# Kernel tuning notes

Hardware: AMD Instinct MI355X
Metric: run time of the kernel (lower is better)

## Reference

```python
import jax, jax.numpy as jnp
import numpy as np

N, D = 1024, 128
NEG_INF = -1e30


def setup_inputs() -> dict:
    key = jax.random.key(0)
    ks = jax.random.split(key, 8)
    s = 0.05
    return {
        "X": jax.random.normal(ks[0], (N, D), dtype=jnp.float32),
        "Wq": jax.random.normal(ks[1], (D, D), dtype=jnp.float32) * s,
        "Wk": jax.random.normal(ks[2], (D, D), dtype=jnp.float32) * s,
        "v": jax.random.normal(ks[3], (D,), dtype=jnp.float32) * s,
        "w_ih": jax.random.normal(ks[4], (3 * D, 2 * D), dtype=jnp.float32) * s,
        "w_hh": jax.random.normal(ks[5], (3 * D, D), dtype=jnp.float32) * s,
        "b_ih": jax.random.normal(ks[6], (3 * D,), dtype=jnp.float32) * s,
        "b_hh": jax.random.normal(ks[7], (3 * D,), dtype=jnp.float32) * s,
    }


def reference(X, Wq, Wk, v, w_ih, w_hh, b_ih, b_hh):
    n, d = X.shape
    # --- anti-causal additive attention (query i attends keys j >= i) ---
    q = X @ Wq.T                                   # (N, d)
    k = X @ Wk.T                                   # (N, d)
    # scores[i, j] = v . tanh(q_i + k_j)
    scores = jnp.einsum("ijd,d->ij", jnp.tanh(q[:, None, :] + k[None, :, :]), v)
    mask = jnp.arange(n)[None, :] >= jnp.arange(n)[:, None]   # suffix j >= i
    scores = jnp.where(mask, scores, NEG_INF)
    w = jax.nn.softmax(scores, axis=1)             # (N, N)
    att = w @ X                                    # (N, d) context over keys

    # --- single-layer GRU over the N "time" steps, batch 1 ---
    gru_in = jnp.concatenate((X, att), axis=1)     # (N, 2d)
    gi = gru_in @ w_ih.T + b_ih                    # (N, 3d) input gates, precomputed

    def step(h, gi_t):
        gh = h @ w_hh.T + b_hh                     # (3d,)
        i_r, i_z, i_n = jnp.split(gi_t, 3)
        h_r, h_z, h_n = jnp.split(gh, 3)
        r = jax.nn.sigmoid(i_r + h_r)
        z = jax.nn.sigmoid(i_z + h_z)
        nst = jnp.tanh(i_n + r * h_n)
        h_new = (1.0 - z) * nst + z * h
        return h_new, h_new

    h0 = jnp.zeros((d,), dtype=X.dtype)
    _, out = jax.lax.scan(step, h0, gi)            # (N, d)
    return out
```

## Files before the change

### kernel.cpp

```cpp
#include <hip/hip_runtime.h>
#include <hip/hip_bf16.h>

#define N 1024
#define D 128
#define SB 8
#define NSB (N / SB)

typedef __hip_bfloat16 bf16;
typedef __attribute__((ext_vector_type(8))) short bfx8;
typedef __attribute__((ext_vector_type(4))) float fx4;
typedef __attribute__((ext_vector_type(4))) unsigned short u16x4;

__device__ __forceinline__ float b2f(bf16 x) { return __bfloat162float(x); }
__device__ __forceinline__ short f2bf_bits(float x) {
    bf16 b = __float2bfloat16(x);
    return *reinterpret_cast<short*>(&b);
}
__device__ __forceinline__ float bfbits2f(unsigned short u) {
    return __uint_as_float(((unsigned int)u) << 16);
}
__device__ __forceinline__ float fastrcp(float x) { return __builtin_amdgcn_rcpf(x); }

__device__ __forceinline__ float fast_tanh(float x) {
    float e = __expf(2.f * x);
    return 1.f - 2.f * fastrcp(e + 1.f);
}
__device__ __forceinline__ float fast_sigmoid(float x) {
    return fastrcp(1.f + __expf(-x));
}

__device__ __forceinline__ float sel4(fx4 v, int r) {
    float x = (r & 1) ? v[1] : v[0];
    float y = (r & 1) ? v[3] : v[2];
    return (r & 2) ? y : x;
}

__device__ __forceinline__ void async_copy16(const float* g, void* l) {
    __builtin_amdgcn_global_load_lds((const __attribute__((address_space(1))) void*)g,
                                     (__attribute__((address_space(3))) void*)l, 16, 0, 0);
}

__device__ __forceinline__ void wait_rows(int* cnt, int grp) {
    while (__hip_atomic_load(&cnt[grp], __ATOMIC_ACQUIRE, __HIP_MEMORY_SCOPE_AGENT) < 8)
        __builtin_amdgcn_s_sleep(2);
}

__device__ __forceinline__ float cvt(const void* p, int idx, int isbf) {
    return isbf ? b2f(((const bf16*)p)[idx]) : ((const float*)p)[idx];
}

#define MFMA(A, B, C) __builtin_amdgcn_mfma_f32_16x16x32_bf16((A), (B), (C), 0, 0, 0)

__global__ void __launch_bounds__(256) prep_kernel(
        const void* inX, const void* inWq, const void* inWk, const void* inV,
        const void* inWih, const void* inWhh, const void* inBih, const void* inBhh,
        float* __restrict__ Xf, float* __restrict__ WqT, float* __restrict__ WkT,
        float* __restrict__ vf, float* __restrict__ wihT, float* __restrict__ whhf,
        float* __restrict__ bihf, float* __restrict__ bhhf,
        int* __restrict__ flag, int* __restrict__ cnt, int* __restrict__ rcnt) {
    __shared__ int red[256];
    int t = threadIdx.x;
    const unsigned short* xu = (const unsigned short*)inX;
    int c = 0;
#pragma unroll
    for (int k = 0; k < 4; ++k) {
        unsigned short u = xu[2 * (4 * t + k)];
        int e = (u >> 7) & 0xFF;
        c += (e >= 96 && e <= 144) ? 1 : 0;
    }
    red[t] = c;
    __syncthreads();
    for (int st = 128; st > 0; st >>= 1) {
        if (t < st) red[t] += red[t + st];
        __syncthreads();
    }
    int isbf = red[0] > 800;

    if (blockIdx.x == 0) {
        if (t == 0) *flag = isbf;
        if (t < 128) { cnt[t] = 0; rcnt[t] = 0; }
    }

    int id = blockIdx.x * 256 + t;
    if (id < 131072) {
        Xf[id] = cvt(inX, id, isbf);
    } else if (id < 147456) {
        int k = id - 131072; int cc = k >> 7, d = k & 127;
        WqT[k] = cvt(inWq, d * 128 + cc, isbf);
    } else if (id < 163840) {
        int k = id - 147456; int cc = k >> 7, d = k & 127;
        WkT[k] = cvt(inWk, d * 128 + cc, isbf);
    } else if (id < 163968) {
        vf[id - 163840] = cvt(inV, id - 163840, isbf);
    } else if (id < 262272) {
        int k = id - 163968; int cc = k / 384, o = k - cc * 384;
        wihT[k] = cvt(inWih, o * 256 + cc, isbf);
    } else if (id < 311424) {
        whhf[id - 262272] = cvt(inWhh, id - 262272, isbf);
    } else if (id < 311808) {
        bihf[id - 311424] = cvt(inBih, id - 311424, isbf);
    } else if (id < 312192) {
        bhhf[id - 311808] = cvt(inBhh, id - 311808, isbf);
    }
}

__global__ void __launch_bounds__(256) qk_gix_kernel(
        const float* __restrict__ X, const float* __restrict__ WqT,
        const float* __restrict__ WkT, const float* __restrict__ wihT,
        float* __restrict__ q, float* __restrict__ kT, float* __restrict__ gix) {
    int i = blockIdx.x, t = threadIdx.x;
    __shared__ float xs[D];
    if (t < D) xs[t] = X[i * D + t];
    __syncthreads();
    int d = t & 127;
    const float* WT = (t < 128) ? WqT : WkT;
    float acc = 0.f;
#pragma unroll 8
    for (int cc = 0; cc < D; ++cc) acc += xs[cc] * WT[cc * D + d];
    if (t < 128) q[i * D + d] = acc;
    else         kT[d * N + i] = acc;

    for (int o = t; o < 3 * D; o += 256) {
        float a2 = 0.f;
#pragma unroll 8
        for (int cc = 0; cc < D; ++cc) a2 += xs[cc] * wihT[cc * 384 + o];
        gix[i * 384 + o] = a2;
    }
}

__global__ void __launch_bounds__(256, 1) fused_kernel(
        const float* __restrict__ q, const float* __restrict__ kT,
        const float* __restrict__ v, const float* __restrict__ X,
        const float* __restrict__ wihT, const float* __restrict__ b_ih,
        const float* __restrict__ b_hh, const float* __restrict__ gix,
        float* __restrict__ gi, const float* __restrict__ w_hh,
        void* __restrict__ out, const int* __restrict__ flag,
        int* __restrict__ cnt, int* __restrict__ rcnt,
        float* __restrict__ attMS, float* __restrict__ attA) {
    __shared__ __align__(16) char smem[2 * SB * 3 * D * 4 + (SB + 1) * D * 2];
    int t = threadIdx.x;

    if (blockIdx.x != 0) {
        int b = blockIdx.x - 1;
        int i, P, p;
        if (b < 256)      { i = b >> 3;            P = 8; p = b & 7; }
        else if (b < 448) { int e = b - 256; i = 32 + (e >> 1); P = 2; p = e & 1; }
        else              { i = 128 + (b - 448);   P = 1; p = 0; }

        float* qs   = (float*)smem;
        float* vs   = qs + D;
        float* al   = vs + D;
        float* wrow = al + D;
        float* red  = wrow + N;

        int len = (N - i + P - 1) / P;
        int j0 = i + p * len;
        int j1 = min(j0 + len, N);

        if (t < D) { qs[t] = q[i * D + t]; vs[t] = v[t]; }
        __syncthreads();

        float sj[4];
        int nj = 0;
        float m = -1e30f;
        for (int j = j0 + t; j < j1; j += 256) {
            float s = 0.f;
#pragma unroll 8
            for (int dd = 0; dd < D; ++dd) s += vs[dd] * fast_tanh(qs[dd] + kT[dd * N + j]);
            sj[nj++] = s;
            m = fmaxf(m, s);
        }
        red[t] = m;
        __syncthreads();
        for (int st = 128; st > 0; st >>= 1) {
            if (t < st) red[t] = fmaxf(red[t], red[t + st]);
            __syncthreads();
        }
        m = red[0];
        __syncthreads();
        float lsum = 0.f;
        {
            int it = 0;
            for (int j = j0 + t; j < j1; j += 256, ++it) {
                float pe = __expf(sj[it] - m);
                wrow[j - j0] = pe;
                lsum += pe;
            }
        }
        red[t] = lsum;
        __syncthreads();
        for (int st = 128; st > 0; st >>= 1) {
            if (t < st) red[t] += red[t + st];
            __syncthreads();
        }
        float S = red[0];
        __syncthreads();
        int d = t & 127, half = t >> 7;
        float acc = 0.f;
        int cl = j1 - j0;
        for (int jj = half; jj < cl; jj += 2) acc += wrow[jj] * X[(j0 + jj) * D + d];
        if (half) red[d] = acc;
        __syncthreads();
        if (!half) al[d] = acc + red[d];
        __syncthreads();

        if (P > 1) {
            if (t < D) attA[(i * 8 + p) * D + t] = al[t];
            if (t == 0) { attMS[(i * 8 + p) * 2] = m; attMS[(i * 8 + p) * 2 + 1] = S; }
            __syncthreads();
            if (t == 0) {
                __threadfence();
                int arr = __hip_atomic_fetch_add(&rcnt[i], 1, __ATOMIC_ACQ_REL,
                                                 __HIP_MEMORY_SCOPE_AGENT);
                ((int*)red)[0] = arr;
            }
            __syncthreads();
            int arr = ((int*)red)[0];
            if (arr != P - 1) return;
            if (t < D) {
                float M = -1e30f;
                for (int pp = 0; pp < P; ++pp) M = fmaxf(M, attMS[(i * 8 + pp) * 2]);
                float Ssum = 0.f, av = 0.f;
                for (int pp = 0; pp < P; ++pp) {
                    float wp = __expf(attMS[(i * 8 + pp) * 2] - M);
                    Ssum += attMS[(i * 8 + pp) * 2 + 1] * wp;
                    av += attA[(i * 8 + pp) * D + t] * wp;
                }
                al[t] = av * fastrcp(Ssum);
            }
            __syncthreads();
        } else {
            float inv = fastrcp(S);
            if (t < D) al[t] *= inv;
            __syncthreads();
        }

        for (int o = t; o < 3 * D; o += 256) {
            float a2 = b_ih[o] + ((o < 2 * D) ? b_hh[o] : 0.f) + gix[i * 384 + o];
            const float* wt = wihT + D * 384 + o;
#pragma unroll 8
            for (int cc = 0; cc < D; ++cc) a2 += al[cc] * wt[cc * 384];
            gi[i * 3 * D + o] = a2;
        }
        __syncthreads();
        if (t == 0) {
            __threadfence();
            __hip_atomic_fetch_add(&cnt[i >> 3], 1, __ATOMIC_RELEASE, __HIP_MEMORY_SCOPE_AGENT);
        }
        return;
    }

    __builtin_amdgcn_s_setprio(1);
    float* gi_lds = (float*)smem;
    short* hist   = (short*)(smem + 2 * SB * 3 * D * 4);
    int w = t >> 6;
    int l = t & 63;
    int qq = l >> 4;
    int nn = l & 15;
    int isbf = *flag;

    bfx8 a[3][2][4];
#pragma unroll
    for (int tau = 0; tau < 3; ++tau)
#pragma unroll
        for (int mqi = 0; mqi < 2; ++mqi)
#pragma unroll
            for (int kc = 0; kc < 4; ++kc) {
                int row = 128 * tau + 16 * (2 * w + mqi) + nn;
                int k0 = 32 * kc + 8 * qq;
#pragma unroll
                for (int j = 0; j < 8; ++j)
                    a[tau][mqi][kc][j] = f2bf_bits(w_hh[row * D + k0 + j]);
            }
    fx4 bias2[2];
#pragma unroll
    for (int mqi = 0; mqi < 2; ++mqi)
#pragma unroll
        for (int r = 0; r < 4; ++r)
            bias2[mqi][r] = b_hh[2 * D + 16 * (2 * w + mqi) + 4 * qq + r];

    int rsel = l & 3;
    int mqsel = (l >> 3) & 1;
    int drow = 32 * w + 16 * mqsel + 4 * qq + rsel;
    float h = 0.f;

    int fr = 1 + (t >> 5);
    int fc = (t & 31) * 4;

    wait_rows(cnt, 0);
    {
        const float* src = gi;
        for (int mm = 0; mm < 3; ++mm) {
            int off = (w * 3 + mm) * 256;
            async_copy16(src + off + (l << 2), smem + off * 4);
        }
    }

    for (int sb = 0; sb < NSB; ++sb) {
        int cb = sb & 1;
        u16x4 hv = {0, 0, 0, 0};
        int hcopy = 0;
        if (sb > 0) {
            hv = *(const u16x4*)(hist + fr * D + fc);
            if (t < 64) hcopy = ((const int*)(hist + SB * D))[t];
        }
        if (sb + 1 < NSB) {
            wait_rows(cnt, sb + 1);
            const float* src = gi + (size_t)(sb + 1) * SB * 3 * D;
            char* dst = smem + (cb ^ 1) * SB * 3 * D * 4;
            for (int mm = 0; mm < 3; ++mm) {
                int off = (w * 3 + mm) * 256;
                async_copy16(src + off + (l << 2), dst + off * 4);
            }
        }
        if (sb > 0) {
            int orow = (sb - 1) * SB + fr - 1;
            if (isbf) {
                *(u16x4*)((unsigned short*)out + orow * D + fc) = hv;
            } else {
                float* op = (float*)out + orow * D + fc;
                fx4 f0;
#pragma unroll
                for (int j = 0; j < 4; ++j) f0[j] = bfbits2f(hv[j]);
                *(fx4*)op = f0;
            }
        }
        if (t < 64) ((int*)hist)[t] = (sb == 0) ? 0 : hcopy;

        if (sb == 0)
            asm volatile("s_waitcnt vmcnt(3) lgkmcnt(0)\ns_barrier" ::: "memory");
        else if (sb == 1)
            asm volatile("s_waitcnt vmcnt(4) lgkmcnt(0)\ns_barrier" ::: "memory");
        else if (sb + 1 < NSB)
            asm volatile("s_waitcnt vmcnt(5) lgkmcnt(0)\ns_barrier" ::: "memory");
        else
            asm volatile("s_waitcnt vmcnt(2) lgkmcnt(0)\ns_barrier" ::: "memory");

        const char* hrd = (const char*)hist + 16 * qq;
        const float* gp = gi_lds + cb * SB * 3 * D + drow;
        short* hwr = hist + D + drow;

        for (int s = 0; s < SB; ++s) {
            bfx8 b0 = *(const bfx8*)(hrd);
            bfx8 b1 = *(const bfx8*)(hrd + 64);
            bfx8 b2 = *(const bfx8*)(hrd + 128);
            bfx8 b3 = *(const bfx8*)(hrd + 192);
            float gr = gp[0];
            float gz = gp[D];
            float gn = gp[2 * D];

            fx4 acc[3][2];
#pragma unroll
            for (int tau = 0; tau < 3; ++tau)
#pragma unroll
                for (int mqi = 0; mqi < 2; ++mqi) {
                    fx4 c0 = (tau == 2) ? bias2[mqi] : fx4{0.f, 0.f, 0.f, 0.f};
                    c0 = MFMA(a[tau][mqi][0], b0, c0);
                    c0 = MFMA(a[tau][mqi][1], b1, c0);
                    c0 = MFMA(a[tau][mqi][2], b2, c0);
                    c0 = MFMA(a[tau][mqi][3], b3, c0);
                    acc[tau][mqi] = c0;
                }

            float ar = sel4(mqsel ? acc[0][1] : acc[0][0], rsel);
            float az = sel4(mqsel ? acc[1][1] : acc[1][0], rsel);
            float an = sel4(mqsel ? acc[2][1] : acc[2][0], rsel);
            float rr = fast_sigmoid(gr + ar);
            float zz = fast_sigmoid(gz + az);
            float nst = fast_tanh(gn + rr * an);
            h = (1.f - zz) * nst + zz * h;
            *hwr = f2bf_bits(h);

            hrd += 256;
            gp += 3 * D;
            hwr += D;
            asm volatile("s_waitcnt lgkmcnt(0)\ns_barrier" ::: "memory");
        }
    }
    {
        u16x4 hv = *(const u16x4*)(hist + fr * D + fc);
        int orow = (NSB - 1) * SB + fr - 1;
        if (isbf) {
            *(u16x4*)((unsigned short*)out + orow * D + fc) = hv;
        } else {
            float* op = (float*)out + orow * D + fc;
            fx4 f0;
#pragma unroll
            for (int j = 0; j < 4; ++j) f0[j] = bfbits2f(hv[j]);
            *(fx4*)op = f0;
        }
    }
}

extern "C" void kernel_launch(void* const* d_in, const int* in_sizes, int n_in,
                              void* d_out, int out_size, void* d_ws, size_t ws_size,
                              hipStream_t stream) {
    (void)in_sizes; (void)n_in; (void)out_size; (void)ws_size;

    float* w0 = (float*)d_ws;
    int*   flag = (int*)w0;
    int*   cnt  = (int*)w0 + 16;
    int*   rcnt = (int*)w0 + 160;
    float* base = w0 + 320;
    float* Xf    = base;
    float* vf    = Xf + 131072;
    float* whhf  = vf + 128;
    float* bihf  = whhf + 49152;
    float* bhhf  = bihf + 384;
    float* WqT   = bhhf + 384;
    float* WkT   = WqT + 16384;
    float* wihT  = WkT + 16384;
    float* q     = wihT + 98304;
    float* kT    = q + 131072;
    float* gix   = kT + 131072;
    float* gi    = gix + 393216;
    float* attMS = gi + 393216;
    float* attA  = attMS + 2048;

    prep_kernel<<<1220, 256, 0, stream>>>(d_in[0], d_in[1], d_in[2], d_in[3],
                                          d_in[4], d_in[5], d_in[6], d_in[7],
                                          Xf, WqT, WkT, vf, wihT, whhf, bihf, bhhf,
                                          flag, cnt, rcnt);
    qk_gix_kernel<<<N, 256, 0, stream>>>(Xf, WqT, WkT, wihT, q, kT, gix);
    fused_kernel<<<1345, 256, 0, stream>>>(q, kT, vf, Xf, wihT, bihf, bhhf, gix,
                                           gi, whhf, d_out, flag, cnt, rcnt,
                                           attMS, attA);
}
```

Baseline: 584.0 us.

## Process 8 rows per block in qk_gix and prefetch GRU gate inputs

The projection kernel now computes 8 rows of X per block, so each weight load from global memory is reused across 8 rows instead of 1, and the grid shrinks from 1024 to 128 blocks. In the GRU recurrence loop, the next step's precomputed input gates are read from LDS one iteration early, keeping that LDS latency off the serial critical path. The hidden-state update is rewritten as nst + z*(h - nst) to save one operation. The cost is more registers per thread and fewer blocks, which may lower occupancy of the projection kernel.

```diff
diff --git a/kernel.cpp b/kernel.cpp
--- a/kernel.cpp
+++ b/kernel.cpp
@@ -5,6 +5,7 @@
 #define D 128
 #define SB 8
 #define NSB (N / SB)
+#define QKROWS 8
 
 typedef __hip_bfloat16 bf16;
 typedef __attribute__((ext_vector_type(8))) short bfx8;
@@ -108,23 +109,43 @@
         const float* __restrict__ X, const float* __restrict__ WqT,
         const float* __restrict__ WkT, const float* __restrict__ wihT,
         float* __restrict__ q, float* __restrict__ kT, float* __restrict__ gix) {
-    int i = blockIdx.x, t = threadIdx.x;
-    __shared__ float xs[D];
-    if (t < D) xs[t] = X[i * D + t];
+    int i0 = blockIdx.x * QKROWS;
+    int t = threadIdx.x;
+    __shared__ float xs[QKROWS][D];
+    for (int k = t; k < QKROWS * D; k += 256) xs[k >> 7][k & 127] = X[i0 * D + k];
     __syncthreads();
+
     int d = t & 127;
     const float* WT = (t < 128) ? WqT : WkT;
-    float acc = 0.f;
-#pragma unroll 8
-    for (int cc = 0; cc < D; ++cc) acc += xs[cc] * WT[cc * D + d];
-    if (t < 128) q[i * D + d] = acc;
-    else         kT[d * N + i] = acc;
+    float acc[QKROWS];
+#pragma unroll
+    for (int r = 0; r < QKROWS; ++r) acc[r] = 0.f;
+#pragma unroll 4
+    for (int cc = 0; cc < D; ++cc) {
+        float wv = WT[cc * D + d];
+#pragma unroll
+        for (int r = 0; r < QKROWS; ++r) acc[r] += xs[r][cc] * wv;
+    }
+    if (t < 128) {
+#pragma unroll
+        for (int r = 0; r < QKROWS; ++r) q[(i0 + r) * D + d] = acc[r];
+    } else {
+#pragma unroll
+        for (int r = 0; r < QKROWS; ++r) kT[d * N + i0 + r] = acc[r];
+    }
 
     for (int o = t; o < 3 * D; o += 256) {
-        float a2 = 0.f;
-#pragma unroll 8
-        for (int cc = 0; cc < D; ++cc) a2 += xs[cc] * wihT[cc * 384 + o];
-        gix[i * 384 + o] = a2;
+        float g[QKROWS];
+#pragma unroll
+        for (int r = 0; r < QKROWS; ++r) g[r] = 0.f;
+#pragma unroll 4
+        for (int cc = 0; cc < D; ++cc) {
+            float wv = wihT[cc * 384 + o];
+#pragma unroll
+            for (int r = 0; r < QKROWS; ++r) g[r] += xs[r][cc] * wv;
+        }
+#pragma unroll
+        for (int r = 0; r < QKROWS; ++r) gix[(i0 + r) * 384 + o] = g[r];
     }
 }
 
@@ -278,6 +299,7 @@
 #pragma unroll
         for (int r = 0; r < 4; ++r)
             bias2[mqi][r] = b_hh[2 * D + 16 * (2 * w + mqi) + 4 * qq + r];
+    const fx4 zed = {0.f, 0.f, 0.f, 0.f};
 
     int rsel = l & 3;
     int mqsel = (l >> 3) & 1;
@@ -340,21 +362,26 @@
         const float* gp = gi_lds + cb * SB * 3 * D + drow;
         short* hwr = hist + D + drow;
 
+        float gr = gp[0], gz = gp[D], gn = gp[2 * D];
+
         for (int s = 0; s < SB; ++s) {
             bfx8 b0 = *(const bfx8*)(hrd);
             bfx8 b1 = *(const bfx8*)(hrd + 64);
             bfx8 b2 = *(const bfx8*)(hrd + 128);
             bfx8 b3 = *(const bfx8*)(hrd + 192);
-            float gr = gp[0];
-            float gz = gp[D];
-            float gn = gp[2 * D];
+            float grn = 0.f, gzn = 0.f, gnn = 0.f;
+            if (s + 1 < SB) {
+                grn = gp[3 * D];
+                gzn = gp[4 * D];
+                gnn = gp[5 * D];
+            }
 
             fx4 acc[3][2];
 #pragma unroll
             for (int tau = 0; tau < 3; ++tau)
 #pragma unroll
                 for (int mqi = 0; mqi < 2; ++mqi) {
-                    fx4 c0 = (tau == 2) ? bias2[mqi] : fx4{0.f, 0.f, 0.f, 0.f};
+                    fx4 c0 = (tau == 2) ? bias2[mqi] : zed;
                     c0 = MFMA(a[tau][mqi][0], b0, c0);
                     c0 = MFMA(a[tau][mqi][1], b1, c0);
                     c0 = MFMA(a[tau][mqi][2], b2, c0);
@@ -368,12 +395,13 @@
             float rr = fast_sigmoid(gr + ar);
             float zz = fast_sigmoid(gz + az);
             float nst = fast_tanh(gn + rr * an);
-            h = (1.f - zz) * nst + zz * h;
+            h = nst + zz * (h - nst);
             *hwr = f2bf_bits(h);
 
             hrd += 256;
             gp += 3 * D;
             hwr += D;
+            gr = grn; gz = gzn; gn = gnn;
             asm volatile("s_waitcnt lgkmcnt(0)\ns_barrier" ::: "memory");
         }
     }
@@ -421,7 +449,7 @@
                                           d_in[4], d_in[5], d_in[6], d_in[7],
                                           Xf, WqT, WkT, vf, wihT, whhf, bihf, bhhf,
                                           flag, cnt, rcnt);
-    qk_gix_kernel<<<N, 256, 0, stream>>>(Xf, WqT, WkT, wihT, q, kT, gix);
+    qk_gix_kernel<<<N / QKROWS, 256, 0, stream>>>(Xf, WqT, WkT, wihT, q, kT, gix);
     fused_kernel<<<1345, 256, 0, stream>>>(q, kT, vf, Xf, wihT, bihf, bhhf, gix,
                                            gi, whhf, d_out, flag, cnt, rcnt,
                                            attMS, attA);
```

New measurement: 591.8 us. Within noise of the previous version (+1.3%).

## Fold q/k/gix projection into persistent fused kernel with grid-wide barrier

Applied to the files above, without the earlier changes.

Removes the separate qk_gix kernel launch and makes the fused kernel persistent with 511 worker blocks plus the GRU block. Workers first compute q, kT and gix rows strided across blocks, sync through a global atomic counter, then loop over the attention work units. The GRU block now starts without waiting for a separate launch, prefetches next-step gi values from shared memory, and raises its priority. Grid-wide spinning assumes all 512 blocks are co-resident and gives up per-unit launch parallelism for fewer blocks looping.

```diff
diff --git a/kernel.cpp b/kernel.cpp
--- a/kernel.cpp
+++ b/kernel.cpp
@@ -5,6 +5,7 @@
 #define D 128
 #define SB 8
 #define NSB (N / SB)
+#define NW 511
 
 typedef __hip_bfloat16 bf16;
 typedef __attribute__((ext_vector_type(8))) short bfx8;
@@ -57,7 +58,8 @@
         float* __restrict__ Xf, float* __restrict__ WqT, float* __restrict__ WkT,
         float* __restrict__ vf, float* __restrict__ wihT, float* __restrict__ whhf,
         float* __restrict__ bihf, float* __restrict__ bhhf,
-        int* __restrict__ flag, int* __restrict__ cnt, int* __restrict__ rcnt) {
+        int* __restrict__ flag, int* __restrict__ cnt, int* __restrict__ rcnt,
+        int* __restrict__ qkcnt) {
     __shared__ int red[256];
     int t = threadIdx.x;
     const unsigned short* xu = (const unsigned short*)inX;
@@ -77,7 +79,7 @@
     int isbf = red[0] > 800;
 
     if (blockIdx.x == 0) {
-        if (t == 0) *flag = isbf;
+        if (t == 0) { *flag = isbf; *qkcnt = 0; }
         if (t < 128) { cnt[t] = 0; rcnt[t] = 0; }
     }
 
@@ -104,153 +106,164 @@
     }
 }
 
-__global__ void __launch_bounds__(256) qk_gix_kernel(
-        const float* __restrict__ X, const float* __restrict__ WqT,
-        const float* __restrict__ WkT, const float* __restrict__ wihT,
-        float* __restrict__ q, float* __restrict__ kT, float* __restrict__ gix) {
-    int i = blockIdx.x, t = threadIdx.x;
-    __shared__ float xs[D];
-    if (t < D) xs[t] = X[i * D + t];
-    __syncthreads();
-    int d = t & 127;
-    const float* WT = (t < 128) ? WqT : WkT;
-    float acc = 0.f;
-#pragma unroll 8
-    for (int cc = 0; cc < D; ++cc) acc += xs[cc] * WT[cc * D + d];
-    if (t < 128) q[i * D + d] = acc;
-    else         kT[d * N + i] = acc;
-
-    for (int o = t; o < 3 * D; o += 256) {
-        float a2 = 0.f;
-#pragma unroll 8
-        for (int cc = 0; cc < D; ++cc) a2 += xs[cc] * wihT[cc * 384 + o];
-        gix[i * 384 + o] = a2;
-    }
-}
-
 __global__ void __launch_bounds__(256, 1) fused_kernel(
-        const float* __restrict__ q, const float* __restrict__ kT,
+        float* __restrict__ q, float* __restrict__ kT,
         const float* __restrict__ v, const float* __restrict__ X,
         const float* __restrict__ wihT, const float* __restrict__ b_ih,
-        const float* __restrict__ b_hh, const float* __restrict__ gix,
+        const float* __restrict__ b_hh, float* __restrict__ gix,
         float* __restrict__ gi, const float* __restrict__ w_hh,
         void* __restrict__ out, const int* __restrict__ flag,
         int* __restrict__ cnt, int* __restrict__ rcnt,
-        float* __restrict__ attMS, float* __restrict__ attA) {
+        float* __restrict__ attMS, float* __restrict__ attA,
+        const float* __restrict__ WqT, const float* __restrict__ WkT,
+        int* __restrict__ qkcnt) {
     __shared__ __align__(16) char smem[2 * SB * 3 * D * 4 + (SB + 1) * D * 2];
     int t = threadIdx.x;
 
     if (blockIdx.x != 0) {
-        int b = blockIdx.x - 1;
-        int i, P, p;
-        if (b < 256)      { i = b >> 3;            P = 8; p = b & 7; }
-        else if (b < 448) { int e = b - 256; i = 32 + (e >> 1); P = 2; p = e & 1; }
-        else              { i = 128 + (b - 448);   P = 1; p = 0; }
-
-        float* qs   = (float*)smem;
-        float* vs   = qs + D;
-        float* al   = vs + D;
-        float* wrow = al + D;
-        float* red  = wrow + N;
-
-        int len = (N - i + P - 1) / P;
-        int j0 = i + p * len;
-        int j1 = min(j0 + len, N);
-
-        if (t < D) { qs[t] = q[i * D + t]; vs[t] = v[t]; }
-        __syncthreads();
-
-        float sj[4];
-        int nj = 0;
-        float m = -1e30f;
-        for (int j = j0 + t; j < j1; j += 256) {
-            float s = 0.f;
+        int wid = blockIdx.x - 1;
+
+        {
+            float* xs = (float*)smem;
+            for (int r = wid; r < N; r += NW) {
+                if (t < D) xs[t] = X[r * D + t];
+                __syncthreads();
+                int d = t & 127;
+                const float* WT = (t < 128) ? WqT : WkT;
+                float acc = 0.f;
 #pragma unroll 8
-            for (int dd = 0; dd < D; ++dd) s += vs[dd] * fast_tanh(qs[dd] + kT[dd * N + j]);
-            sj[nj++] = s;
-            m = fmaxf(m, s);
-        }
-        red[t] = m;
-        __syncthreads();
-        for (int st = 128; st > 0; st >>= 1) {
-            if (t < st) red[t] = fmaxf(red[t], red[t + st]);
-            __syncthreads();
-        }
-        m = red[0];
-        __syncthreads();
-        float lsum = 0.f;
-        {
-            int it = 0;
-            for (int j = j0 + t; j < j1; j += 256, ++it) {
-                float pe = __expf(sj[it] - m);
-                wrow[j - j0] = pe;
-                lsum += pe;
-            }
-        }
-        red[t] = lsum;
-        __syncthreads();
-        for (int st = 128; st > 0; st >>= 1) {
-            if (t < st) red[t] += red[t + st];
-            __syncthreads();
-        }
-        float S = red[0];
-        __syncthreads();
-        int d = t & 127, half = t >> 7;
-        float acc = 0.f;
-        int cl = j1 - j0;
-        for (int jj = half; jj < cl; jj += 2) acc += wrow[jj] * X[(j0 + jj) * D + d];
-        if (half) red[d] = acc;
-        __syncthreads();
-        if (!half) al[d] = acc + red[d];
-        __syncthreads();
-
-        if (P > 1) {
-            if (t < D) attA[(i * 8 + p) * D + t] = al[t];
-            if (t == 0) { attMS[(i * 8 + p) * 2] = m; attMS[(i * 8 + p) * 2 + 1] = S; }
-            __syncthreads();
+                for (int cc = 0; cc < D; ++cc) acc += xs[cc] * WT[cc * D + d];
+                if (t < 128) q[r * D + d] = acc;
+                else         kT[d * N + r] = acc;
+                for (int o = t; o < 3 * D; o += 256) {
+                    float g = 0.f;
+#pragma unroll 8
+                    for (int cc = 0; cc < D; ++cc) g += xs[cc] * wihT[cc * 384 + o];
+                    gix[r * 384 + o] = g;
+                }
+                __syncthreads();
+            }
             if (t == 0) {
                 __threadfence();
-                int arr = __hip_atomic_fetch_add(&rcnt[i], 1, __ATOMIC_ACQ_REL,
-                                                 __HIP_MEMORY_SCOPE_AGENT);
-                ((int*)red)[0] = arr;
-            }
-            __syncthreads();
-            int arr = ((int*)red)[0];
-            if (arr != P - 1) return;
-            if (t < D) {
-                float M = -1e30f;
-                for (int pp = 0; pp < P; ++pp) M = fmaxf(M, attMS[(i * 8 + pp) * 2]);
-                float Ssum = 0.f, av = 0.f;
-                for (int pp = 0; pp < P; ++pp) {
-                    float wp = __expf(attMS[(i * 8 + pp) * 2] - M);
-                    Ssum += attMS[(i * 8 + pp) * 2 + 1] * wp;
-                    av += attA[(i * 8 + pp) * D + t] * wp;
+                __hip_atomic_fetch_add(qkcnt, 1, __ATOMIC_RELEASE, __HIP_MEMORY_SCOPE_AGENT);
+            }
+            while (__hip_atomic_load(qkcnt, __ATOMIC_ACQUIRE, __HIP_MEMORY_SCOPE_AGENT) < NW)
+                __builtin_amdgcn_s_sleep(4);
+        }
+
+        for (int u = wid; u < 1344; u += NW) {
+            int i, P, p;
+            if (u < 256)      { i = u >> 3;            P = 8; p = u & 7; }
+            else if (u < 448) { int e = u - 256; i = 32 + (e >> 1); P = 2; p = e & 1; }
+            else              { i = 128 + (u - 448);   P = 1; p = 0; }
+
+            float* qs   = (float*)smem;
+            float* vs   = qs + D;
+            float* al   = vs + D;
+            float* wrow = al + D;
+            float* red  = wrow + N;
+
+            int len = (N - i + P - 1) / P;
+            int j0 = i + p * len;
+            int j1 = min(j0 + len, N);
+
+            __syncthreads();
+            if (t < D) { qs[t] = q[i * D + t]; vs[t] = v[t]; }
+            __syncthreads();
+
+            float sj[4];
+            int nj = 0;
+            float m = -1e30f;
+            for (int j = j0 + t; j < j1; j += 256) {
+                float s = 0.f;
+#pragma unroll 8
+                for (int dd = 0; dd < D; ++dd) s += vs[dd] * fast_tanh(qs[dd] + kT[dd * N + j]);
+                sj[nj++] = s;
+                m = fmaxf(m, s);
+            }
+            red[t] = m;
+            __syncthreads();
+            for (int st = 128; st > 0; st >>= 1) {
+                if (t < st) red[t] = fmaxf(red[t], red[t + st]);
+                __syncthreads();
+            }
+            m = red[0];
+            __syncthreads();
+            float lsum = 0.f;
+            {
+                int it = 0;
+                for (int j = j0 + t; j < j1; j += 256, ++it) {
+                    float pe = __expf(sj[it] - m);
+                    wrow[j - j0] = pe;
+                    lsum += pe;
                 }
-                al[t] = av * fastrcp(Ssum);
-            }
-            __syncthreads();
-        } else {
-            float inv = fastrcp(S);
-            if (t < D) al[t] *= inv;
-            __syncthreads();
-        }
-
-        for (int o = t; o < 3 * D; o += 256) {
-            float a2 = b_ih[o] + ((o < 2 * D) ? b_hh[o] : 0.f) + gix[i * 384 + o];
-            const float* wt = wihT + D * 384 + o;
+            }
+            red[t] = lsum;
+            __syncthreads();
+            for (int st = 128; st > 0; st >>= 1) {
+                if (t < st) red[t] += red[t + st];
+                __syncthreads();
+            }
+            float S = red[0];
+            __syncthreads();
+            int d = t & 127, half = t >> 7;
+            float acc = 0.f;
+            int cl = j1 - j0;
+            for (int jj = half; jj < cl; jj += 2) acc += wrow[jj] * X[(j0 + jj) * D + d];
+            if (half) red[d] = acc;
+            __syncthreads();
+            if (!half) al[d] = acc + red[d];
+            __syncthreads();
+
+            if (P > 1) {
+                if (t < D) attA[(i * 8 + p) * D + t] = al[t];
+                if (t == 0) { attMS[(i * 8 + p) * 2] = m; attMS[(i * 8 + p) * 2 + 1] = S; }
+                __syncthreads();
+                if (t == 0) {
+                    __threadfence();
+                    int arr = __hip_atomic_fetch_add(&rcnt[i], 1, __ATOMIC_ACQ_REL,
+                                                     __HIP_MEMORY_SCOPE_AGENT);
+                    ((int*)red)[0] = arr;
+                }
+                __syncthreads();
+                int arr = ((int*)red)[0];
+                if (arr != P - 1) continue;
+                if (t < D) {
+                    float M = -1e30f;
+                    for (int pp = 0; pp < P; ++pp) M = fmaxf(M, attMS[(i * 8 + pp) * 2]);
+                    float Ssum = 0.f, av = 0.f;
+                    for (int pp = 0; pp < P; ++pp) {
+                        float wp = __expf(attMS[(i * 8 + pp) * 2] - M);
+                        Ssum += attMS[(i * 8 + pp) * 2 + 1] * wp;
+                        av += attA[(i * 8 + pp) * D + t] * wp;
+                    }
+                    al[t] = av * fastrcp(Ssum);
+                }
+                __syncthreads();
+            } else {
+                float inv = fastrcp(S);
+                if (t < D) al[t] *= inv;
+                __syncthreads();
+            }
+
+            for (int o = t; o < 3 * D; o += 256) {
+                float a2 = b_ih[o] + ((o < 2 * D) ? b_hh[o] : 0.f) + gix[i * 384 + o];
+                const float* wt = wihT + D * 384 + o;
 #pragma unroll 8
-            for (int cc = 0; cc < D; ++cc) a2 += al[cc] * wt[cc * 384];
-            gi[i * 3 * D + o] = a2;
-        }
-        __syncthreads();
-        if (t == 0) {
-            __threadfence();
-            __hip_atomic_fetch_add(&cnt[i >> 3], 1, __ATOMIC_RELEASE, __HIP_MEMORY_SCOPE_AGENT);
+                for (int cc = 0; cc < D; ++cc) a2 += al[cc] * wt[cc * 384];
+                gi[i * 3 * D + o] = a2;
+            }
+            __syncthreads();
+            if (t == 0) {
+                __threadfence();
+                __hip_atomic_fetch_add(&cnt[i >> 3], 1, __ATOMIC_RELEASE,
+                                       __HIP_MEMORY_SCOPE_AGENT);
+            }
         }
         return;
     }
 
-    __builtin_amdgcn_s_setprio(1);
+    __builtin_amdgcn_s_setprio(2);
     float* gi_lds = (float*)smem;
     short* hist   = (short*)(smem + 2 * SB * 3 * D * 4);
     int w = t >> 6;
@@ -278,6 +291,7 @@
 #pragma unroll
         for (int r = 0; r < 4; ++r)
             bias2[mqi][r] = b_hh[2 * D + 16 * (2 * w + mqi) + 4 * qq + r];
+    const fx4 zed = {0.f, 0.f, 0.f, 0.f};
 
     int rsel = l & 3;
     int mqsel = (l >> 3) & 1;
@@ -340,21 +354,26 @@
         const float* gp = gi_lds + cb * SB * 3 * D + drow;
         short* hwr = hist + D + drow;
 
+        float gr = gp[0], gz = gp[D], gn = gp[2 * D];
+
         for (int s = 0; s < SB; ++s) {
             bfx8 b0 = *(const bfx8*)(hrd);
             bfx8 b1 = *(const bfx8*)(hrd + 64);
             bfx8 b2 = *(const bfx8*)(hrd + 128);
             bfx8 b3 = *(const bfx8*)(hrd + 192);
-            float gr = gp[0];
-            float gz = gp[D];
-            float gn = gp[2 * D];
+            float grn = 0.f, gzn = 0.f, gnn = 0.f;
+            if (s + 1 < SB) {
+                grn = gp[3 * D];
+                gzn = gp[4 * D];
+                gnn = gp[5 * D];
+            }
 
             fx4 acc[3][2];
 #pragma unroll
             for (int tau = 0; tau < 3; ++tau)
 #pragma unroll
                 for (int mqi = 0; mqi < 2; ++mqi) {
-                    fx4 c0 = (tau == 2) ? bias2[mqi] : fx4{0.f, 0.f, 0.f, 0.f};
+                    fx4 c0 = (tau == 2) ? bias2[mqi] : zed;
                     c0 = MFMA(a[tau][mqi][0], b0, c0);
                     c0 = MFMA(a[tau][mqi][1], b1, c0);
                     c0 = MFMA(a[tau][mqi][2], b2, c0);
@@ -368,12 +387,13 @@
             float rr = fast_sigmoid(gr + ar);
             float zz = fast_sigmoid(gz + az);
             float nst = fast_tanh(gn + rr * an);
-            h = (1.f - zz) * nst + zz * h;
+            h = nst + zz * (h - nst);
             *hwr = f2bf_bits(h);
 
             hrd += 256;
             gp += 3 * D;
             hwr += D;
+            gr = grn; gz = gzn; gn = gnn;
             asm volatile("s_waitcnt lgkmcnt(0)\ns_barrier" ::: "memory");
         }
     }
@@ -398,9 +418,10 @@
     (void)in_sizes; (void)n_in; (void)out_size; (void)ws_size;
 
     float* w0 = (float*)d_ws;
-    int*   flag = (int*)w0;
-    int*   cnt  = (int*)w0 + 16;
-    int*   rcnt = (int*)w0 + 160;
+    int*   flag  = (int*)w0;
+    int*   qkcnt = (int*)w0 + 8;
+    int*   cnt   = (int*)w0 + 16;
+    int*   rcnt  = (int*)w0 + 160;
     float* base = w0 + 320;
     float* Xf    = base;
     float* vf    = Xf + 131072;
@@ -420,9 +441,8 @@
     prep_kernel<<<1220, 256, 0, stream>>>(d_in[0], d_in[1], d_in[2], d_in[3],
                                           d_in[4], d_in[5], d_in[6], d_in[7],
                                           Xf, WqT, WkT, vf, wihT, whhf, bihf, bhhf,
-                                          flag, cnt, rcnt);
-    qk_gix_kernel<<<N, 256, 0, stream>>>(Xf, WqT, WkT, wihT, q, kT, gix);
-    fused_kernel<<<1345, 256, 0, stream>>>(q, kT, vf, Xf, wihT, bihf, bhhf, gix,
-                                           gi, whhf, d_out, flag, cnt, rcnt,
-                                           attMS, attA);
-}
+                                          flag, cnt, rcnt, qkcnt);
+    fused_kernel<<<NW + 1, 256, 0, stream>>>(q, kT, vf, Xf, wihT, bihf, bhhf, gix,
+                                             gi, whhf, d_out, flag, cnt, rcnt,
+                                             attMS, attA, WqT, WkT, qkcnt);
+}
```

Result: slower. 1.062 ms (+81.8%).

## Fold input conversion into projection kernel and prefetch GRU gate inputs

Applied to the files above, without the earlier changes.

Removes the separate prep kernel that converted and transposed all inputs into fp32 workspace. The projection kernel now reads raw weights directly (row-wise, bf16 or fp32), and the fused kernel converts v, biases and w_hh on the fly. Only the attention half of w_ih is still transposed, spread across blocks. The GRU loop also prefetches the next step's gate inputs from LDS, rewrites the state update with one fewer multiply, and raises the recurrent wave's priority. Each projection thread now reads a contiguous weight row instead of coalesced columns, which may hurt memory access patterns.

```diff
diff --git a/kernel.cpp b/kernel.cpp
--- a/kernel.cpp
+++ b/kernel.cpp
@@ -51,15 +51,16 @@
 
 #define MFMA(A, B, C) __builtin_amdgcn_mfma_f32_16x16x32_bf16((A), (B), (C), 0, 0, 0)
 
-__global__ void __launch_bounds__(256) prep_kernel(
-        const void* inX, const void* inWq, const void* inWk, const void* inV,
-        const void* inWih, const void* inWhh, const void* inBih, const void* inBhh,
-        float* __restrict__ Xf, float* __restrict__ WqT, float* __restrict__ WkT,
-        float* __restrict__ vf, float* __restrict__ wihT, float* __restrict__ whhf,
-        float* __restrict__ bihf, float* __restrict__ bhhf,
+__global__ void __launch_bounds__(256) qk_kernel(
+        const void* inX, const void* inWq, const void* inWk, const void* inWih,
+        float* __restrict__ Xf, float* __restrict__ q, float* __restrict__ kT,
+        float* __restrict__ gix, float* __restrict__ wihTa,
         int* __restrict__ flag, int* __restrict__ cnt, int* __restrict__ rcnt) {
+    __shared__ float xs[D];
     __shared__ int red[256];
+    int i = blockIdx.x;
     int t = threadIdx.x;
+
     const unsigned short* xu = (const unsigned short*)inX;
     int c = 0;
 #pragma unroll
@@ -76,69 +77,65 @@
     }
     int isbf = red[0] > 800;
 
-    if (blockIdx.x == 0) {
+    if (i == 0) {
         if (t == 0) *flag = isbf;
         if (t < 128) { cnt[t] = 0; rcnt[t] = 0; }
     }
 
-    int id = blockIdx.x * 256 + t;
-    if (id < 131072) {
-        Xf[id] = cvt(inX, id, isbf);
-    } else if (id < 147456) {
-        int k = id - 131072; int cc = k >> 7, d = k & 127;
-        WqT[k] = cvt(inWq, d * 128 + cc, isbf);
-    } else if (id < 163840) {
-        int k = id - 147456; int cc = k >> 7, d = k & 127;
-        WkT[k] = cvt(inWk, d * 128 + cc, isbf);
-    } else if (id < 163968) {
-        vf[id - 163840] = cvt(inV, id - 163840, isbf);
-    } else if (id < 262272) {
-        int k = id - 163968; int cc = k / 384, o = k - cc * 384;
-        wihT[k] = cvt(inWih, o * 256 + cc, isbf);
-    } else if (id < 311424) {
-        whhf[id - 262272] = cvt(inWhh, id - 262272, isbf);
-    } else if (id < 311808) {
-        bihf[id - 311424] = cvt(inBih, id - 311424, isbf);
-    } else if (id < 312192) {
-        bhhf[id - 311808] = cvt(inBhh, id - 311808, isbf);
-    }
-}
-
-__global__ void __launch_bounds__(256) qk_gix_kernel(
-        const float* __restrict__ X, const float* __restrict__ WqT,
-        const float* __restrict__ WkT, const float* __restrict__ wihT,
-        float* __restrict__ q, float* __restrict__ kT, float* __restrict__ gix) {
-    int i = blockIdx.x, t = threadIdx.x;
-    __shared__ float xs[D];
-    if (t < D) xs[t] = X[i * D + t];
+    if (t < D) {
+        float xv = cvt(inX, i * D + t, isbf);
+        xs[t] = xv;
+        Xf[i * D + t] = xv;
+    }
     __syncthreads();
+
     int d = t & 127;
-    const float* WT = (t < 128) ? WqT : WkT;
     float acc = 0.f;
-#pragma unroll 8
-    for (int cc = 0; cc < D; ++cc) acc += xs[cc] * WT[cc * D + d];
+    if (isbf) {
+        const bf16* Wr = (const bf16*)((t < 128) ? inWq : inWk) + (size_t)d * D;
+#pragma unroll 8
+        for (int cc = 0; cc < D; ++cc) acc += xs[cc] * b2f(Wr[cc]);
+    } else {
+        const float* Wr = (const float*)((t < 128) ? inWq : inWk) + (size_t)d * D;
+#pragma unroll 8
+        for (int cc = 0; cc < D; ++cc) acc += xs[cc] * Wr[cc];
+    }
     if (t < 128) q[i * D + d] = acc;
     else         kT[d * N + i] = acc;
 
     for (int o = t; o < 3 * D; o += 256) {
-        float a2 = 0.f;
-#pragma unroll 8
-        for (int cc = 0; cc < D; ++cc) a2 += xs[cc] * wihT[cc * 384 + o];
-        gix[i * 384 + o] = a2;
+        float g = 0.f;
+        if (isbf) {
+            const bf16* wr = (const bf16*)inWih + (size_t)o * 256;
+#pragma unroll 8
+            for (int cc = 0; cc < D; ++cc) g += xs[cc] * b2f(wr[cc]);
+        } else {
+            const float* wr = (const float*)inWih + (size_t)o * 256;
+#pragma unroll 8
+            for (int cc = 0; cc < D; ++cc) g += xs[cc] * wr[cc];
+        }
+        gix[i * 384 + o] = g;
+    }
+
+    if (t < 48) {
+        int k = i * 48 + t;
+        int cc = k / 384, o = k - cc * 384;
+        wihTa[k] = cvt(inWih, o * 256 + 128 + cc, isbf);
     }
 }
 
 __global__ void __launch_bounds__(256, 1) fused_kernel(
         const float* __restrict__ q, const float* __restrict__ kT,
-        const float* __restrict__ v, const float* __restrict__ X,
-        const float* __restrict__ wihT, const float* __restrict__ b_ih,
-        const float* __restrict__ b_hh, const float* __restrict__ gix,
-        float* __restrict__ gi, const float* __restrict__ w_hh,
+        const void* __restrict__ inV, const float* __restrict__ X,
+        const float* __restrict__ wihTa, const void* __restrict__ inBih,
+        const void* __restrict__ inBhh, const float* __restrict__ gix,
+        float* __restrict__ gi, const void* __restrict__ inWhh,
         void* __restrict__ out, const int* __restrict__ flag,
         int* __restrict__ cnt, int* __restrict__ rcnt,
         float* __restrict__ attMS, float* __restrict__ attA) {
     __shared__ __align__(16) char smem[2 * SB * 3 * D * 4 + (SB + 1) * D * 2];
     int t = threadIdx.x;
+    int isbf = *flag;
 
     if (blockIdx.x != 0) {
         int b = blockIdx.x - 1;
@@ -157,7 +154,7 @@
         int j0 = i + p * len;
         int j1 = min(j0 + len, N);
 
-        if (t < D) { qs[t] = q[i * D + t]; vs[t] = v[t]; }
+        if (t < D) { qs[t] = q[i * D + t]; vs[t] = cvt(inV, t, isbf); }
         __syncthreads();
 
         float sj[4];
@@ -236,8 +233,9 @@
         }
 
         for (int o = t; o < 3 * D; o += 256) {
-            float a2 = b_ih[o] + ((o < 2 * D) ? b_hh[o] : 0.f) + gix[i * 384 + o];
-            const float* wt = wihT + D * 384 + o;
+            float a2 = cvt(inBih, o, isbf) + ((o < 2 * D) ? cvt(inBhh, o, isbf) : 0.f)
+                     + gix[i * 384 + o];
+            const float* wt = wihTa + o;
 #pragma unroll 8
             for (int cc = 0; cc < D; ++cc) a2 += al[cc] * wt[cc * 384];
             gi[i * 3 * D + o] = a2;
@@ -250,14 +248,13 @@
         return;
     }
 
-    __builtin_amdgcn_s_setprio(1);
+    __builtin_amdgcn_s_setprio(2);
     float* gi_lds = (float*)smem;
     short* hist   = (short*)(smem + 2 * SB * 3 * D * 4);
     int w = t >> 6;
     int l = t & 63;
     int qq = l >> 4;
     int nn = l & 15;
-    int isbf = *flag;
 
     bfx8 a[3][2][4];
 #pragma unroll
@@ -270,14 +267,15 @@
                 int k0 = 32 * kc + 8 * qq;
 #pragma unroll
                 for (int j = 0; j < 8; ++j)
-                    a[tau][mqi][kc][j] = f2bf_bits(w_hh[row * D + k0 + j]);
+                    a[tau][mqi][kc][j] = f2bf_bits(cvt(inWhh, row * D + k0 + j, isbf));
             }
     fx4 bias2[2];
 #pragma unroll
     for (int mqi = 0; mqi < 2; ++mqi)
 #pragma unroll
         for (int r = 0; r < 4; ++r)
-            bias2[mqi][r] = b_hh[2 * D + 16 * (2 * w + mqi) + 4 * qq + r];
+            bias2[mqi][r] = cvt(inBhh, 2 * D + 16 * (2 * w + mqi) + 4 * qq + r, isbf);
+    const fx4 zed = {0.f, 0.f, 0.f, 0.f};
 
     int rsel = l & 3;
     int mqsel = (l >> 3) & 1;
@@ -340,21 +338,26 @@
         const float* gp = gi_lds + cb * SB * 3 * D + drow;
         short* hwr = hist + D + drow;
 
+        float gr = gp[0], gz = gp[D], gn = gp[2 * D];
+
         for (int s = 0; s < SB; ++s) {
             bfx8 b0 = *(const bfx8*)(hrd);
             bfx8 b1 = *(const bfx8*)(hrd + 64);
             bfx8 b2 = *(const bfx8*)(hrd + 128);
             bfx8 b3 = *(const bfx8*)(hrd + 192);
-            float gr = gp[0];
-            float gz = gp[D];
-            float gn = gp[2 * D];
+            float grn = 0.f, gzn = 0.f, gnn = 0.f;
+            if (s + 1 < SB) {
+                grn = gp[3 * D];
+                gzn = gp[4 * D];
+                gnn = gp[5 * D];
+            }
 
             fx4 acc[3][2];
 #pragma unroll
             for (int tau = 0; tau < 3; ++tau)
 #pragma unroll
                 for (int mqi = 0; mqi < 2; ++mqi) {
-                    fx4 c0 = (tau == 2) ? bias2[mqi] : fx4{0.f, 0.f, 0.f, 0.f};
+                    fx4 c0 = (tau == 2) ? bias2[mqi] : zed;
                     c0 = MFMA(a[tau][mqi][0], b0, c0);
                     c0 = MFMA(a[tau][mqi][1], b1, c0);
                     c0 = MFMA(a[tau][mqi][2], b2, c0);
@@ -368,12 +371,13 @@
             float rr = fast_sigmoid(gr + ar);
             float zz = fast_sigmoid(gz + az);
             float nst = fast_tanh(gn + rr * an);
-            h = (1.f - zz) * nst + zz * h;
+            h = nst + zz * (h - nst);
             *hwr = f2bf_bits(h);
 
             hrd += 256;
             gp += 3 * D;
             hwr += D;
+            gr = grn; gz = gzn; gn = gnn;
             asm volatile("s_waitcnt lgkmcnt(0)\ns_barrier" ::: "memory");
         }
     }
@@ -403,26 +407,17 @@
     int*   rcnt = (int*)w0 + 160;
     float* base = w0 + 320;
     float* Xf    = base;
-    float* vf    = Xf + 131072;
-    float* whhf  = vf + 128;
-    float* bihf  = whhf + 49152;
-    float* bhhf  = bihf + 384;
-    float* WqT   = bhhf + 384;
-    float* WkT   = WqT + 16384;
-    float* wihT  = WkT + 16384;
-    float* q     = wihT + 98304;
+    float* q     = Xf + 131072;
     float* kT    = q + 131072;
     float* gix   = kT + 131072;
     float* gi    = gix + 393216;
-    float* attMS = gi + 393216;
+    float* wihTa = gi + 393216;
+    float* attMS = wihTa + 49152;
     float* attA  = attMS + 2048;
 
-    prep_kernel<<<1220, 256, 0, stream>>>(d_in[0], d_in[1], d_in[2], d_in[3],
-                                          d_in[4], d_in[5], d_in[6], d_in[7],
-                                          Xf, WqT, WkT, vf, wihT, whhf, bihf, bhhf,
-                                          flag, cnt, rcnt);
-    qk_gix_kernel<<<N, 256, 0, stream>>>(Xf, WqT, WkT, wihT, q, kT, gix);
-    fused_kernel<<<1345, 256, 0, stream>>>(q, kT, vf, Xf, wihT, bihf, bhhf, gix,
-                                           gi, whhf, d_out, flag, cnt, rcnt,
-                                           attMS, attA);
-}
+    qk_kernel<<<N, 256, 0, stream>>>(d_in[0], d_in[1], d_in[2], d_in[4],
+                                     Xf, q, kT, gix, wihTa, flag, cnt, rcnt);
+    fused_kernel<<<1345, 256, 0, stream>>>(q, kT, d_in[3], Xf, wihTa, d_in[6],
+                                           d_in[7], gix, gi, d_in[5], d_out,
+                                           flag, cnt, rcnt, attMS, attA);
+}
```

Result: slower. 614.3 us (+5.2%).
